# Kernel tuning notes

Hardware: AMD Instinct MI355X
Metric: run time of the kernel (lower is better)

The kernel has to match this reference:

```python
import jax, jax.numpy as jnp
import numpy as np

N_AGENTS = 32
N_HEADS = 8
HEAD_DIM = 32          # atten_dim // n_heads
HID = 256              # rnn_hidden_dim
ATT = 256              # atten_dim
N_ACT = 32
NEG = -1e9             # finite stand-in for -inf; exp underflows to 0 in softmax


def setup_inputs() -> dict:
    key = jax.random.key(0)
    ks = jax.random.split(key, 20)
    B, N, E = 4096, 64, 128
    w = lambda k, shape: (jax.random.normal(k, shape, jnp.float32) * 0.05)
    return {
        "inputs": jax.random.normal(ks[0], (B, N, E), jnp.float32),
        "hidden_state": jax.random.normal(ks[1], (B, N_AGENTS, HID), jnp.float32) * 0.1,
        "fc1_w": w(ks[2], (HID, E)), "fc1_b": jnp.zeros((HID,), jnp.float32),
        "q_w": w(ks[3], (ATT, HID)), "q_b": jnp.zeros((ATT,), jnp.float32),
        "k_w": w(ks[4], (ATT, HID)), "k_b": jnp.zeros((ATT,), jnp.float32),
        "v_w": w(ks[5], (ATT, HID)), "v_b": jnp.zeros((ATT,), jnp.float32),
        "w_ih": w(ks[6], (3 * HID, ATT)), "w_hh": w(ks[7], (3 * HID, HID)),
        "b_ih": jnp.zeros((3 * HID,), jnp.float32), "b_hh": jnp.zeros((3 * HID,), jnp.float32),
        "out_w": w(ks[8], (N_ACT, HID)), "out_b": jnp.zeros((N_ACT,), jnp.float32),
        "obs_mask": jax.random.randint(ks[9], (B, N, N), 0, 2).astype(bool),
        "scenario_mask": jax.random.randint(ks[10], (B, N_AGENTS), 0, 2).astype(bool),
    }


def reference(inputs, hidden_state, fc1_w, fc1_b, q_w, q_b, k_w, k_b, v_w, v_b,
              w_ih, w_hh, b_ih, b_hh, out_w, out_b, obs_mask, scenario_mask):
    B, N, _ = inputs.shape
    A, nh, e = N_AGENTS, N_HEADS, HEAD_DIM
    # fc1 + ReLU: [B, N, HID]
    x = jax.nn.relu(inputs @ fc1_w.T + fc1_b)
    # multi-head projections; queries only for the first A entities (agents)
    q = (x[:, :A] @ q_w.T + q_b).reshape(B, A, nh, e).transpose(0, 2, 1, 3)   # [B,nh,A,e]
    k = (x @ k_w.T + k_b).reshape(B, N, nh, e).transpose(0, 2, 3, 1)          # [B,nh,e,N]
    v = jax.nn.relu(x @ v_w.T + v_b).reshape(B, N, nh, e).transpose(0, 2, 1, 3)  # [B,nh,N,e]
    score = jnp.einsum('bhae,bhen->bhan', q, k) / np.float32(np.sqrt(e))      # [B,nh,A,N]
    m = obs_mask[:, :A, :][:, None, :, :]                                      # [B,1,A,N]
    score = jnp.where(m, NEG, score)
    w = jax.nn.softmax(score, axis=-1)
    # original: fully-masked rows give NaN then are zeroed; here zero all masked slots
    w = jnp.where(m, 0.0, w)
    att = jnp.einsum('bhan,bhne->bhae', w, v)                                  # [B,nh,A,e]
    att = att.transpose(0, 2, 1, 3).reshape(B * A, nh * e)                     # [B*A, ATT]
    # GRUCell step (PyTorch gate ordering: r, z, n)
    h0 = hidden_state.reshape(B * A, HID)
    gi = att @ w_ih.T + b_ih
    gh = h0 @ w_hh.T + b_hh
    ir, iz, in_ = jnp.split(gi, 3, axis=-1)
    hr, hz, hn = jnp.split(gh, 3, axis=-1)
    r = jax.nn.sigmoid(ir + hr)
    z = jax.nn.sigmoid(iz + hz)
    n = jnp.tanh(in_ + r * hn)
    h = (1.0 - z) * n + z * h0
    h = h.reshape(B, A, HID)
    am = scenario_mask[:, :, None]                                             # [B,A,1]
    h = jnp.where(am, 0.0, h)
    q_out = h @ out_w.T + out_b
    q_out = jnp.where(am, 0.0, q_out)
    return q_out, h
```

## Files before the change

kernel.cpp:

```cpp
#include <hip/hip_runtime.h>


using bfrag = __attribute__((ext_vector_type(8))) short;
using s4    = __attribute__((ext_vector_type(4))) short;
using ffrag = __attribute__((ext_vector_type(4))) float;

#define MFMA(a,b,c) __builtin_amdgcn_mfma_f32_16x16x32_bf16((a),(b),(c),0,0,0)
#define SWZ(row,col,S,xm) ((row)*(S) + ((((col)&~7) ^ (((row)&(xm))<<3)) | ((col)&7)))

#define OFF_A2   0L
#define OFF_FC1  67108864L
#define OFF_QKV  67141632L
#define OFF_W6   67338240L
#define OFF_OW   67731456L
#define OFF_FLAG 67739648L
#define WS_NEED_BYTES 135479552L

__device__ inline unsigned short f2bf(float x){
  union { float f; unsigned u; } v; v.f = x;
  unsigned r = v.u + 0x7fffu + ((v.u >> 16) & 1u);
  return (unsigned short)(r >> 16);
}
__device__ inline bool getmask(const void* p, long i, int byteflag){
  return byteflag ? (((const unsigned char*)p)[i] != 0)
                  : (((const int*)p)[i] != 0);
}
__device__ inline ffrag fzero(){ ffrag z; z[0]=0.f; z[1]=0.f; z[2]=0.f; z[3]=0.f; return z; }
__device__ inline void gload16(const short* g, short* l){
  __builtin_amdgcn_global_load_lds((const __attribute__((address_space(1))) void*)g,
                                   (__attribute__((address_space(3))) void*)l, 16, 0, 0);
}
__device__ inline bfrag packbf(const float* p){
  float4 f0 = *(const float4*)p; float4 f1 = *(const float4*)(p+4);
  bfrag v;
  v[0]=(short)f2bf(f0.x); v[1]=(short)f2bf(f0.y); v[2]=(short)f2bf(f0.z); v[3]=(short)f2bf(f0.w);
  v[4]=(short)f2bf(f1.x); v[5]=(short)f2bf(f1.y); v[6]=(short)f2bf(f1.z); v[7]=(short)f2bf(f1.w);
  return v;
}

__global__ void k0_prep(const float* __restrict__ fc1, const float* __restrict__ qw,
    const float* __restrict__ kw, const float* __restrict__ vw, const float* __restrict__ wih,
    const float* __restrict__ whh, const float* __restrict__ ow,
    const void* __restrict__ obsm, short* __restrict__ ws){
  long tid = (long)blockIdx.x*blockDim.x + threadIdx.x;
  long n = (long)gridDim.x*blockDim.x;
  if (tid == 0){
    const int* mi = (const int*)obsm;
    int f = 0;
    for (int i=0;i<256;i++){ if ((unsigned)mi[i] > 1u){ f = 1; break; } }
    ((int*)(ws + OFF_FLAG))[0] = f;
  }
  for (long i=tid; i<32768; i+=n){
    int R = (int)(i>>7), c = (int)(i&127);
    int seg = R>>6, r = R&63;
    ws[OFF_FC1 + ((long)(seg*64+r)<<7) + (c ^ ((r&7)<<3))] = (short)f2bf(fc1[i]);
  }
  for (long i=tid; i<65536; i+=n){
    int R = (int)(i>>8), C = (int)(i&255);
    int cb = R>>6, r = R&63;
    int cs = C ^ ((r&7)<<3);
    long base = (long)cb*16384 + (long)r*256 + cs;
    ws[OFF_QKV + 0L*65536 + base] = (short)f2bf(qw[i]);
    ws[OFF_QKV + 1L*65536 + base] = (short)f2bf(kw[i]);
    ws[OFF_QKV + 2L*65536 + base] = (short)f2bf(vw[i]);
  }
  for (long i=tid; i<196608; i+=n){
    int gate = (int)(i >> 16);
    int grow = (int)((i >> 8) & 255);
    int c = (int)(i & 255);
    int jb = grow >> 5, row = grow & 31;
    int cs = c ^ ((row&7)<<3);
    ws[OFF_W6 + ((long)((jb*6 + gate)*32 + row))*256 + cs]     = (short)f2bf(wih[i]);
    ws[OFF_W6 + ((long)((jb*6 + 3 + gate)*32 + row))*256 + cs] = (short)f2bf(whh[i]);
  }
  for (long i=tid; i<8192; i+=n) ws[OFF_OW+i] = (short)f2bf(ow[i]);
}

__global__ __launch_bounds__(512) void k1_fused(const float* __restrict__ inp,
    const short* __restrict__ fc1S, const float* __restrict__ fc1_b,
    const short* __restrict__ qkvS,
    const float* __restrict__ qb, const float* __restrict__ kb, const float* __restrict__ vb,
    const void* __restrict__ obsm, short* __restrict__ A2, const int* __restrict__ flagp){
  __shared__ __align__(16) short smem[75776];
  short* x_s   = smem;
  short* wbuf0 = smem + 16384;
  short* a_s   = smem + 32768;
  short* q_s   = smem + 32768;
  short* k_s   = smem + 40960;
  short* vT_s  = smem + 57344;
  unsigned char* m8 = (unsigned char*)(smem + 73728);
  int t = threadIdx.x; int b = blockIdx.x;
  int lane = t&63, w = t>>6, lr = lane&15, ko = lane>>4;
  int mflag = *flagp;
  auto STG16 = [&](const short* src, short* dst){
    #pragma unroll
    for (int i=0;i<2;i++)
      gload16(src + (long)(i*512 + t)*8, dst + (i*512 + (t&~63))*8);
  };
  auto STG32 = [&](const short* src, short* dst){
    #pragma unroll
    for (int i=0;i<4;i++)
      gload16(src + (long)(i*512 + t)*8, dst + (i*512 + (t&~63))*8);
  };
  STG16(fc1S, wbuf0);
  #pragma unroll
  for (int i=0;i<2;i++){
    int c = t + i*512; int row = c>>4; int cc = (c&15)*8;
    *(bfrag*)(a_s + SWZ(row, cc, 128, 7)) = packbf(inp + ((long)b*64 + row)*128 + cc);
  }
  if (mflag){
    uchar4 mv = *(const uchar4*)((const unsigned char*)obsm + (long)b*4096 + t*4);
    m8[t*4]=mv.x; m8[t*4+1]=mv.y; m8[t*4+2]=mv.z; m8[t*4+3]=mv.w;
  } else {
    int4 mv = *(const int4*)((const int*)obsm + (long)b*4096 + t*4);
    m8[t*4]  =(unsigned char)(mv.x!=0); m8[t*4+1]=(unsigned char)(mv.y!=0);
    m8[t*4+2]=(unsigned char)(mv.z!=0); m8[t*4+3]=(unsigned char)(mv.w!=0);
  }
  __syncthreads();
  {
    int rg1 = w&3, ch1 = w>>2;
    bfrag a1[4];
    #pragma unroll
    for (int ks=0;ks<4;ks++)
      a1[ks] = *(const bfrag*)(a_s + SWZ(rg1*16+lr, ks*32+ko*8, 128, 7));
    for (int s=0;s<4;s++){
      if (s<3) STG16(fc1S + (s+1)*8192, wbuf0 + ((s+1)&1)*8192);
      const short* wc = wbuf0 + (s&1)*8192;
      ffrag acc[2]; acc[0]=fzero(); acc[1]=fzero();
      #pragma unroll
      for (int ks=0;ks<4;ks++){
        int kc = ks*32+ko*8;
        #pragma unroll
        for (int nt=0;nt<2;nt++){
          bfrag bb = *(const bfrag*)(wc + SWZ(ch1*32+nt*16+lr, kc, 128, 7));
          acc[nt] = MFMA(a1[ks], bb, acc[nt]);
        }
      }
      #pragma unroll
      for (int nt=0;nt<2;nt++){
        int colg = s*64 + ch1*32 + nt*16 + lr;
        float bias = fc1_b[colg];
        #pragma unroll
        for (int r=0;r<4;r++){
          int row = rg1*16 + ko*4 + r;
          float v = acc[nt][r] + bias; v = v>0.f?v:0.f;
          x_s[SWZ(row, colg, 256, 7)] = (short)f2bf(v);
        }
      }
      __syncthreads();
    }
  }
  {
    int rg = w&1, chs = w>>1;
    bfrag a_r[2][8];
    #pragma unroll
    for (int mt=0;mt<2;mt++)
      #pragma unroll
      for (int kk=0;kk<8;kk++)
        a_r[mt][kk] = *(const bfrag*)(x_s + SWZ(rg*32+mt*16+lr, kk*32+ko*8, 256, 7));
    STG32(qkvS, wbuf0);
    __syncthreads();
    for (int s=0; s<12; s++){
      if (s<11) STG32(qkvS + (long)(s+1)*16384, ((s+1)&1) ? x_s : wbuf0);
      const short* wc = (s&1) ? x_s : wbuf0;
      int kind = s>>2, cb = s&3;
      bool active = !(kind==0 && rg==1);
      if (active){
        ffrag acc0=fzero(), acc1=fzero();
        #pragma unroll
        for (int ks=0;ks<8;ks++){
          int kc = ks*32+ko*8;
          bfrag bb = *(const bfrag*)(wc + SWZ(chs*16+lr, kc, 256, 7));
          acc0 = MFMA(a_r[0][ks], bb, acc0);
          acc1 = MFMA(a_r[1][ks], bb, acc1);
        }
        int colg = cb*64 + chs*16 + lr;
        if (kind==0){
          float bias = qb[colg];
          #pragma unroll
          for (int r=0;r<4;r++){
            q_s[SWZ(ko*4+r, colg, 256, 7)]    = (short)f2bf(acc0[r] + bias);
            q_s[SWZ(16+ko*4+r, colg, 256, 7)] = (short)f2bf(acc1[r] + bias);
          }
        } else if (kind==1){
          float bias = kb[colg];
          #pragma unroll
          for (int r=0;r<4;r++){
            k_s[SWZ(rg*32+ko*4+r, colg, 256, 7)]    = (short)f2bf(acc0[r] + bias);
            k_s[SWZ(rg*32+16+ko*4+r, colg, 256, 7)] = (short)f2bf(acc1[r] + bias);
          }
        } else {
          float bias = vb[colg];
          int hh = colg>>5, e = colg&31;
          #pragma unroll
          for (int mt=0;mt<2;mt++){
            int n0 = rg*32 + mt*16 + ko*4;
            s4 pk;
            #pragma unroll
            for (int r=0;r<4;r++){
              float v = (mt?acc1[r]:acc0[r]) + bias; v = v>0.f?v:0.f;
              pk[r] = (short)f2bf(v);
            }
            *(s4*)(vT_s + hh*2048 + SWZ(e, n0, 64, 7)) = pk;
          }
        }
      }
      __syncthreads();
    }
  }
  {
    const int h = w;
    short* p_s = wbuf0 + h*2048;
    bfrag a_q[2];
    #pragma unroll
    for (int mt=0; mt<2; mt++)
      a_q[mt] = *(const bfrag*)(q_s + SWZ(mt*16+lr, h*32+ko*8, 256, 7));
    bfrag b_k[4];
    #pragma unroll
    for (int nt=0; nt<4; nt++)
      b_k[nt] = *(const bfrag*)(k_s + SWZ(nt*16+lr, h*32+ko*8, 256, 7));
    ffrag sc[2][4];
    #pragma unroll
    for (int mt=0; mt<2; mt++)
      #pragma unroll
      for (int nt=0; nt<4; nt++) sc[mt][nt] = MFMA(a_q[mt], b_k[nt], fzero());
    const float scale = 0.17677669529663687f;
    float rsi[2][4];
    #pragma unroll
    for (int mt=0; mt<2; mt++){
      #pragma unroll
      for (int r=0; r<4; r++){
        int arow = mt*16 + ko*4 + r;
        float sv[4]; int mk[4];
        #pragma unroll
        for (int nt=0; nt<4; nt++){
          mk[nt] = m8[arow*64 + nt*16 + lr];
          sv[nt] = sc[mt][nt][r] * scale;
        }
        float mx = -3.0e38f;
        #pragma unroll
        for (int nt=0; nt<4; nt++) if (!mk[nt]) mx = fmaxf(mx, sv[nt]);
        for (int d=1; d<16; d<<=1) mx = fmaxf(mx, __shfl_xor(mx, d));
        float sum = 0.f;
        #pragma unroll
        for (int nt=0; nt<4; nt++){
          float p = mk[nt] ? 0.f : __expf(sv[nt]-mx);
          sv[nt] = p; sum += p;
        }
        for (int d=1; d<16; d<<=1) sum += __shfl_xor(sum, d);
        rsi[mt][r] = sum > 0.f ? 1.f/sum : 0.f;
        #pragma unroll
        for (int nt=0; nt<4; nt++)
          p_s[SWZ(arow, nt*16+lr, 64, 7)] = (short)f2bf(sv[nt]);
      }
    }
    ffrag o[2][2];
    #pragma unroll
    for (int mt=0;mt<2;mt++)
      #pragma unroll
      for (int nt=0;nt<2;nt++) o[mt][nt]=fzero();
    #pragma unroll
    for (int kk=0; kk<2; kk++){
      int kc = kk*32 + ko*8;
      bfrag pa0 = *(const bfrag*)(p_s + SWZ(lr,    kc, 64, 7));
      bfrag pa1 = *(const bfrag*)(p_s + SWZ(16+lr, kc, 64, 7));
      bfrag bv0 = *(const bfrag*)(vT_s + h*2048 + SWZ(lr,    kc, 64, 7));
      bfrag bv1 = *(const bfrag*)(vT_s + h*2048 + SWZ(16+lr, kc, 64, 7));
      o[0][0]=MFMA(pa0,bv0,o[0][0]); o[0][1]=MFMA(pa0,bv1,o[0][1]);
      o[1][0]=MFMA(pa1,bv0,o[1][0]); o[1][1]=MFMA(pa1,bv1,o[1][1]);
    }
    #pragma unroll
    for (int mt=0; mt<2; mt++)
      #pragma unroll
      for (int nt=0; nt<2; nt++)
        #pragma unroll
        for (int r=0; r<4; r++){
          int a = mt*16 + ko*4 + r;
          A2[((long)b*32 + a)*256 + h*32 + nt*16 + lr] = (short)f2bf(o[mt][nt][r]*rsi[mt][r]);
        }
  }
}

__global__ __launch_bounds__(512) void k3_gru(const short* __restrict__ A2,
    const float* __restrict__ h0f, const short* __restrict__ w6,
    const float* __restrict__ b_ih, const float* __restrict__ b_hh,
    const void* __restrict__ scen, float* __restrict__ hout, const int* __restrict__ flagp){
  __shared__ __align__(16) short w_s[2][16384];
  int t = threadIdx.x, bid = blockIdx.x;
  long R0 = (long)bid * 128;
  int mflag = *flagp;
  int lane = t&63, w = t>>6, lr = lane&15, ko = lane>>4;
  long rowbase = R0 + (long)w*16;
  auto STAGE = [&](int ph){
    const short* src = w6 + (long)ph*16384;
    short* dst = w_s[ph&1];
    #pragma unroll
    for (int i=0;i<4;i++)
      gload16(src + (long)(i*512 + t)*8, dst + (i*512 + (t & ~63))*8);
  };
  STAGE(0);
  const short* Ab = A2 + (rowbase + lr)*256 + ko*8;
  const float* Hb = h0f + (rowbase + lr)*256 + ko*8;
  bfrag A[16];
  #pragma unroll
  for (int ks=0; ks<8; ks++)
    A[ks] = *(const bfrag*)(Ab + ks*32);
  #pragma unroll
  for (int ks=0; ks<8; ks++)
    A[8+ks] = packbf(Hb + ks*32);
  __syncthreads();
  for (int jb=0; jb<8; jb++){
    ffrag aR[2], aZ[2], aI[2], aN[2];
    #pragma unroll
    for (int nt=0;nt<2;nt++){ aR[nt]=fzero(); aZ[nt]=fzero(); aI[nt]=fzero(); aN[nt]=fzero(); }
    #pragma unroll
    for (int p=0; p<3; p++){
      int ph = jb*3 + p;
      if (ph < 23) STAGE(ph+1);
      const short* wc = w_s[ph&1];
      #pragma unroll
      for (int ks=0; ks<8; ks++){
        int kc = ks*32 + ko*8;
        #pragma unroll
        for (int nt=0; nt<2; nt++){
          bfrag b0 = *(const bfrag*)(wc + SWZ(nt*16+lr, kc, 256, 7));
          bfrag b1 = *(const bfrag*)(wc + 8192 + SWZ(nt*16+lr, kc, 256, 7));
          if (p == 0){
            aR[nt] = MFMA(A[ks], b0, aR[nt]);
            aZ[nt] = MFMA(A[ks], b1, aZ[nt]);
          } else if (p == 1){
            aI[nt] = MFMA(A[ks], b0, aI[nt]);
            aR[nt] = MFMA(A[8+ks], b1, aR[nt]);
          } else {
            aZ[nt] = MFMA(A[8+ks], b0, aZ[nt]);
            aN[nt] = MFMA(A[8+ks], b1, aN[nt]);
          }
        }
      }
      if (p == 2){
        #pragma unroll
        for (int nt=0; nt<2; nt++){
          int j = jb*32 + nt*16 + lr;
          float bir = b_ih[j],     bhr = b_hh[j];
          float biz = b_ih[256+j], bhz = b_hh[256+j];
          float bin = b_ih[512+j], bhn = b_hh[512+j];
          #pragma unroll
          for (int rr=0; rr<4; rr++){
            long row = rowbase + ko*4 + rr;
            float rg = 1.f/(1.f + __expf(-(aR[nt][rr] + bir + bhr)));
            float zg = 1.f/(1.f + __expf(-(aZ[nt][rr] + biz + bhz)));
            float ag = aI[nt][rr] + bin + rg*(aN[nt][rr] + bhn);
            float ng = 2.f/(1.f + __expf(-2.f*ag)) - 1.f;
            float h0v = h0f[row*256 + j];
            float hv = (1.f - zg)*ng + zg*h0v;
            if (getmask(scen, row, mflag)) hv = 0.f;
            hout[row*256 + j] = hv;
          }
        }
      }
      __syncthreads();
    }
  }
}

__global__ __launch_bounds__(512) void k4_out(const float* __restrict__ hout,
    const short* __restrict__ ow, const float* __restrict__ out_b,
    const void* __restrict__ scen, float* __restrict__ qout, const int* __restrict__ flagp){
  __shared__ __align__(16) short ow_s[32*256];
  int t = threadIdx.x; long R0 = (long)blockIdx.x * 256;
  int mflag = *flagp;
  for (int i=0;i<2;i++){
    int c = t + i*512; int row = c >> 5; int cc = (c & 31)*8;
    *(bfrag*)(ow_s + SWZ(row, cc, 256, 7)) = *(const bfrag*)(ow + row*256 + cc);
  }
  __syncthreads();
  int lane = t&63, w = t>>6, lr = lane&15, ko = lane>>4;
  ffrag acc[2][2];
  #pragma unroll
  for (int a=0;a<2;a++) for (int bq=0;bq<2;bq++) acc[a][bq]=fzero();
  for (int ks=0; ks<8; ks++){
    int kc = ks*32 + ko*8;
    #pragma unroll
    for (int mi=0; mi<2; mi++){
      long row = R0 + (w*2+mi)*16 + lr;
      bfrag a = packbf(hout + row*256 + kc);
      #pragma unroll
      for (int nt=0; nt<2; nt++){
        bfrag bb = *(const bfrag*)(ow_s + SWZ(nt*16+lr, kc, 256, 7));
        acc[mi][nt] = MFMA(a, bb, acc[mi][nt]);
      }
    }
  }
  #pragma unroll
  for (int mi=0;mi<2;mi++)
    #pragma unroll
    for (int nt=0;nt<2;nt++){
      int col = nt*16 + lr;
      float ob = out_b[col];
      #pragma unroll
      for (int r=0;r<4;r++){
        long row = R0 + (w*2+mi)*16 + ko*4 + r;
        float qv = acc[mi][nt][r] + ob;
        if (getmask(scen, row, mflag)) qv = 0.f;
        qout[row*32 + col] = qv;
      }
    }
}

extern "C" void kernel_launch(void* const* d_in, const int* in_sizes, int n_in,
                              void* d_out, int out_size, void* d_ws, size_t ws_size,
                              hipStream_t stream){
  const float* inputs = (const float*)d_in[0];
  const float* hidden = (const float*)d_in[1];
  const float* fc1_w  = (const float*)d_in[2];
  const float* fc1_b  = (const float*)d_in[3];
  const float* q_w    = (const float*)d_in[4];
  const float* q_b    = (const float*)d_in[5];
  const float* k_w    = (const float*)d_in[6];
  const float* k_b    = (const float*)d_in[7];
  const float* v_w    = (const float*)d_in[8];
  const float* v_b    = (const float*)d_in[9];
  const float* w_ih   = (const float*)d_in[10];
  const float* w_hh   = (const float*)d_in[11];
  const float* b_ih   = (const float*)d_in[12];
  const float* b_hh   = (const float*)d_in[13];
  const float* out_w  = (const float*)d_in[14];
  const float* out_b  = (const float*)d_in[15];
  const void* obsm    = d_in[16];
  const void* scen    = d_in[17];
  (void)in_sizes; (void)n_in; (void)out_size;
  if ((long)ws_size < WS_NEED_BYTES) return;
  short* ws = (short*)d_ws;
  const int* flagp = (const int*)(ws + OFF_FLAG);
  float* qout = (float*)d_out;
  float* hout = qout + 4194304;
  short* A2  = ws + OFF_A2;

  hipLaunchKernelGGL(k0_prep, dim3(512), dim3(256), 0, stream,
      fc1_w, q_w, k_w, v_w, w_ih, w_hh, out_w, obsm, ws);
  hipLaunchKernelGGL(k1_fused, dim3(4096), dim3(512), 0, stream,
      inputs, ws + OFF_FC1, fc1_b, ws + OFF_QKV, q_b, k_b, v_b, obsm, A2, flagp);
  hipLaunchKernelGGL(k3_gru, dim3(1024), dim3(512), 0, stream,
      A2, hidden, ws + OFF_W6, b_ih, b_hh, scen, hout, flagp);
  hipLaunchKernelGGL(k4_out, dim3(512), dim3(512), 0, stream,
      hout, ws + OFF_OW, out_b, scen, qout, flagp);
}
```

Before: 546.0 us.

## Read fc1/QKV weights directly from global in fragment-major layout, drop LDS staging

Weights are repacked in the prep kernel into an MFMA-fragment-major layout, so each lane loads its B fragment with one contiguous 16-byte global load instead of staging weight tiles through double-buffered LDS. This removes the per-stage weight copies and the per-stage __syncthreads in the fc1 and QKV loops, and cuts LDS use from about 151 KB to about 119 KB. In exchange, every wave now fetches weights from global/L2 memory with no reuse across waves inside the block, so the MFMA loops depend on global-load latency.

Measured after the change: 532.6 us. 2.5% less time.

```diff
diff --git a/kernel.cpp b/kernel.cpp
--- a/kernel.cpp
+++ b/kernel.cpp
@@ -51,18 +51,21 @@
     ((int*)(ws + OFF_FLAG))[0] = f;
   }
   for (long i=tid; i<32768; i+=n){
-    int R = (int)(i>>7), c = (int)(i&127);
-    int seg = R>>6, r = R&63;
-    ws[OFF_FC1 + ((long)(seg*64+r)<<7) + (c ^ ((r&7)<<3))] = (short)f2bf(fc1[i]);
+    int R = (int)(i>>7), C = (int)(i&127);
+    int s = R>>6, colr = R&63, ct = colr>>4, ll = colr&15;
+    int ks = C>>5, rem = C&31, lh = rem>>3, j = rem&7;
+    long dst = ((long)((s*4+ks)*4+ct))*512 + (lh*16+ll)*8 + j;
+    ws[OFF_FC1 + dst] = (short)f2bf(fc1[i]);
   }
   for (long i=tid; i<65536; i+=n){
     int R = (int)(i>>8), C = (int)(i&255);
-    int cb = R>>6, r = R&63;
-    int cs = C ^ ((r&7)<<3);
-    long base = (long)cb*16384 + (long)r*256 + cs;
-    ws[OFF_QKV + 0L*65536 + base] = (short)f2bf(qw[i]);
-    ws[OFF_QKV + 1L*65536 + base] = (short)f2bf(kw[i]);
-    ws[OFF_QKV + 2L*65536 + base] = (short)f2bf(vw[i]);
+    int cb = R>>6, colr = R&63, ct = colr>>4, ll = colr&15;
+    int ks = C>>5, rem = C&31, lh = rem>>3, j = rem&7;
+    long fo = ((long)ks)*4 + ct;
+    long dst = (long)(lh*16+ll)*8 + j + fo*512;
+    ws[OFF_QKV + ((long)(0*4+cb))*16384 + dst] = (short)f2bf(qw[i]);
+    ws[OFF_QKV + ((long)(1*4+cb))*16384 + dst] = (short)f2bf(kw[i]);
+    ws[OFF_QKV + ((long)(2*4+cb))*16384 + dst] = (short)f2bf(vw[i]);
   }
   for (long i=tid; i<196608; i+=n){
     int gate = (int)(i >> 16);
@@ -77,32 +80,20 @@
 }
 
 __global__ __launch_bounds__(512) void k1_fused(const float* __restrict__ inp,
-    const short* __restrict__ fc1S, const float* __restrict__ fc1_b,
-    const short* __restrict__ qkvS,
+    const short* __restrict__ fc1F, const float* __restrict__ fc1_b,
+    const short* __restrict__ qkvF,
     const float* __restrict__ qb, const float* __restrict__ kb, const float* __restrict__ vb,
     const void* __restrict__ obsm, short* __restrict__ A2, const int* __restrict__ flagp){
-  __shared__ __align__(16) short smem[75776];
-  short* x_s   = smem;
-  short* wbuf0 = smem + 16384;
-  short* a_s   = smem + 32768;
-  short* q_s   = smem + 32768;
-  short* k_s   = smem + 40960;
-  short* vT_s  = smem + 57344;
-  unsigned char* m8 = (unsigned char*)(smem + 73728);
+  __shared__ __align__(16) short smem[59392];
+  short* x_s  = smem;
+  short* a_s  = smem + 16384;
+  short* q_s  = smem + 16384;
+  short* k_s  = smem + 24576;
+  short* vT_s = smem + 40960;
+  unsigned char* m8 = (unsigned char*)(smem + 57344);
   int t = threadIdx.x; int b = blockIdx.x;
   int lane = t&63, w = t>>6, lr = lane&15, ko = lane>>4;
   int mflag = *flagp;
-  auto STG16 = [&](const short* src, short* dst){
-    #pragma unroll
-    for (int i=0;i<2;i++)
-      gload16(src + (long)(i*512 + t)*8, dst + (i*512 + (t&~63))*8);
-  };
-  auto STG32 = [&](const short* src, short* dst){
-    #pragma unroll
-    for (int i=0;i<4;i++)
-      gload16(src + (long)(i*512 + t)*8, dst + (i*512 + (t&~63))*8);
-  };
-  STG16(fc1S, wbuf0);
   #pragma unroll
   for (int i=0;i<2;i++){
     int c = t + i*512; int row = c>>4; int cc = (c&15)*8;
@@ -123,16 +114,15 @@
     #pragma unroll
     for (int ks=0;ks<4;ks++)
       a1[ks] = *(const bfrag*)(a_s + SWZ(rg1*16+lr, ks*32+ko*8, 128, 7));
+    #pragma unroll
     for (int s=0;s<4;s++){
-      if (s<3) STG16(fc1S + (s+1)*8192, wbuf0 + ((s+1)&1)*8192);
-      const short* wc = wbuf0 + (s&1)*8192;
       ffrag acc[2]; acc[0]=fzero(); acc[1]=fzero();
       #pragma unroll
       for (int ks=0;ks<4;ks++){
-        int kc = ks*32+ko*8;
         #pragma unroll
         for (int nt=0;nt<2;nt++){
-          bfrag bb = *(const bfrag*)(wc + SWZ(ch1*32+nt*16+lr, kc, 128, 7));
+          int ct = ch1*2 + nt;
+          bfrag bb = *(const bfrag*)(fc1F + ((long)((s*4+ks)*4+ct))*512 + lane*8);
           acc[nt] = MFMA(a1[ks], bb, acc[nt]);
         }
       }
@@ -147,9 +137,9 @@
           x_s[SWZ(row, colg, 256, 7)] = (short)f2bf(v);
         }
       }
-      __syncthreads();
-    }
-  }
+    }
+  }
+  __syncthreads();
   {
     int rg = w&1, chs = w>>1;
     bfrag a_r[2][8];
@@ -158,19 +148,16 @@
       #pragma unroll
       for (int kk=0;kk<8;kk++)
         a_r[mt][kk] = *(const bfrag*)(x_s + SWZ(rg*32+mt*16+lr, kk*32+ko*8, 256, 7));
-    STG32(qkvS, wbuf0);
     __syncthreads();
     for (int s=0; s<12; s++){
-      if (s<11) STG32(qkvS + (long)(s+1)*16384, ((s+1)&1) ? x_s : wbuf0);
-      const short* wc = (s&1) ? x_s : wbuf0;
       int kind = s>>2, cb = s&3;
       bool active = !(kind==0 && rg==1);
       if (active){
+        const short* fb = qkvF + (long)s*16384 + (long)chs*512 + lane*8;
         ffrag acc0=fzero(), acc1=fzero();
         #pragma unroll
         for (int ks=0;ks<8;ks++){
-          int kc = ks*32+ko*8;
-          bfrag bb = *(const bfrag*)(wc + SWZ(chs*16+lr, kc, 256, 7));
+          bfrag bb = *(const bfrag*)(fb + (long)ks*2048);
           acc0 = MFMA(a_r[0][ks], bb, acc0);
           acc1 = MFMA(a_r[1][ks], bb, acc1);
         }
@@ -205,12 +192,12 @@
           }
         }
       }
-      __syncthreads();
-    }
-  }
+    }
+  }
+  __syncthreads();
   {
     const int h = w;
-    short* p_s = wbuf0 + h*2048;
+    short* p_s = x_s + h*2048;
     bfrag a_q[2];
     #pragma unroll
     for (int mt=0; mt<2; mt++)
```
